# Kernel optimization log

Measured on AMD Instinct MI355X. Metric: run time of the kernel, lower is better.

The kernel has to match this reference:

```python
import jax, jax.numpy as jnp
import numpy as np

BORDER = 8
NMS_THRESH = 0.0
NMS_KSIZE = 5
TOP_K = 512
GAUSS_KSIZE = 15
GAUSS_SIGMA = 0.5
LOSS_LAMBDA = 1.0


def filter_border(x, border=BORDER):
    B, C, H, W = x.shape
    mask = jnp.zeros((H, W), x.dtype).at[border:H - border, border:W - border].set(1.0)
    return x * mask


def _bilinear_sample(img, x, y):
    # img: [H,W]; x,y: [H,W] float pixel coords in src frame; zeros outside.
    H, W = img.shape
    x0 = jnp.floor(x)
    y0 = jnp.floor(y)
    wx1 = x - x0
    wy1 = y - y0

    def gather(yy, xx):
        valid = (xx >= 0) & (xx <= W - 1) & (yy >= 0) & (yy <= H - 1)
        xi = jnp.clip(xx, 0, W - 1).astype(jnp.int32)
        yi = jnp.clip(yy, 0, H - 1).astype(jnp.int32)
        return img[yi, xi] * valid.astype(img.dtype)

    return ((1 - wy1) * (1 - wx1) * gather(y0, x0)
            + (1 - wy1) * wx1 * gather(y0, x0 + 1)
            + wy1 * (1 - wx1) * gather(y0 + 1, x0)
            + wy1 * wx1 * gather(y0 + 1, x0 + 1))


def warp_image(ref, src, homo):
    # Sample src at homo-mapped coords of ref's pixel grid -> output in ref frame.
    B, _, H, W = ref.shape
    ys, xs = jnp.meshgrid(jnp.arange(H, dtype=ref.dtype), jnp.arange(W, dtype=ref.dtype), indexing='ij')
    pts = jnp.stack([xs.ravel(), ys.ravel(), jnp.ones(H * W, ref.dtype)], 0)  # [3, HW]
    mapped = jnp.einsum('bij,jn->bin', homo, pts)  # [B,3,HW]
    x = (mapped[:, 0] / mapped[:, 2]).reshape(B, H, W)
    y = (mapped[:, 1] / mapped[:, 2]).reshape(B, H, W)
    out = jax.vmap(_bilinear_sample)(src[:, 0], x, y)  # [B,H,W]
    return out[:, None]


def select_keypoints(score, thresh, ksize, top_k):
    B, _, H, W = score.shape
    pooled = jax.lax.reduce_window(score, -jnp.inf, jax.lax.max,
                                   (1, 1, ksize, ksize), (1, 1, 1, 1), 'SAME')
    keep = (score == pooled) & (score > thresh)
    s = jnp.where(keep, score, 0.0)
    flat = s.reshape(B, H * W)
    vals, idx = jax.lax.top_k(flat, top_k)
    out = jnp.zeros_like(flat).at[jnp.arange(B)[:, None], idx].set(vals)
    kp = jnp.stack([idx // W, idx % W], -1)  # [B, top_k, 2] (y, x)
    return out.reshape(B, 1, H, W), kp


def gaussian_filter(x, ksize, sigma):
    ax = jnp.arange(ksize, dtype=x.dtype) - (ksize - 1) / 2.0
    g = jnp.exp(-(ax ** 2) / (2.0 * sigma ** 2))
    g = g / g.sum()
    k2 = jnp.outer(g, g)[None, None]  # [1,1,k,k]
    return jax.lax.conv_general_dilated(x, k2, (1, 1), 'SAME')


def setup_inputs() -> dict:
    key = jax.random.key(0)
    k1, k2, k3 = jax.random.split(key, 3)
    B, H, W = 16, 480, 640
    score1 = jax.random.uniform(k1, (B, 1, H, W), jnp.float32)
    score2 = jax.random.uniform(k2, (B, 1, H, W), jnp.float32)
    # Near-identity pixel-space homographies: small rotation/shear/perspective + a few px translation.
    scale = jnp.array([[0.01, 0.01, 2.0],
                       [0.01, 0.01, 2.0],
                       [1e-5, 1e-5, 0.0]], jnp.float32)
    homo12 = jnp.eye(3, dtype=jnp.float32) + jax.random.normal(k3, (B, 3, 3), jnp.float32) * scale
    return {"score1": score1, "score2": score2, "homo12": homo12}


def reference(score1, score2, homo12):
    score2 = filter_border(score2)
    w_score2 = warp_image(score1, score2, homo12)
    vis_mask = jnp.ones_like(score2)
    vis_mask1 = (warp_image(score1, vis_mask, homo12) > 0).astype(score1.dtype)
    s1, kp1 = select_keypoints(score1, NMS_THRESH, NMS_KSIZE, TOP_K)
    s1 = gaussian_filter(s1, GAUSS_KSIZE, GAUSS_SIGMA)
    gt_s1, _ = select_keypoints(w_score2, NMS_THRESH, NMS_KSIZE, TOP_K)
    gt_s1 = gaussian_filter(gt_s1, GAUSS_KSIZE, GAUSS_SIGMA)
    norm = vis_mask1.sum()
    loss = (((s1 - gt_s1) ** 2) * vis_mask1 / norm).sum() * LOSS_LAMBDA
    return (loss, kp1, vis_mask1)
```

## Files before the change

kernel.cpp:

```cpp
#include <hip/hip_runtime.h>
#include <cstdint>
#include <cstddef>

#define BN 16
#define HH 480
#define WW 640
#define HWSZ (HH*WW)
#define CAP 32768
#define TOPK 512
#define RED_BLOCKS 2048
#define NTX 64
#define NTY 16

typedef unsigned long long u64;

#define W2_OFF   0ULL
#define W2_SZ    ((unsigned long long)BN*HWSZ*4ULL)
#define MAPS_OFF (W2_OFF + W2_SZ)
#define MAPS_SZ  (2ULL*BN*HWSZ*4ULL)
#define CAND_OFF (MAPS_OFF + MAPS_SZ)
#define CAND_SZ  (2ULL*BN*CAP*8ULL)
#define CNT_OFF  (CAND_OFF + CAND_SZ)
#define CNT_SZ   (4096ULL)
#define SEL_OFF  (CNT_OFF + CNT_SZ)
#define SEL_SZ   (2ULL*BN*TOPK*8ULL)
#define PART_OFF (SEL_OFF + SEL_SZ)
#define PART_SZ  ((unsigned long long)RED_BLOCKS*2*4ULL)

__global__ void k_warp_vis(const float* __restrict__ score2,
                           const float* __restrict__ homo,
                           float* __restrict__ w2,
                           float* __restrict__ vis) {
    int t = blockIdx.x * 256 + threadIdx.x;
    int b = t / (HWSZ / 4);
    int q = t - b * (HWSZ / 4);
    int p = q * 4;
    int py = p / WW, px = p - py * WW;
    const float* h = homo + b * 9;
    const float* sb = score2 + (size_t)b * HWSZ;

    float4 wout;
    float vout[4];
    #pragma unroll
    for (int u = 0; u < 4; ++u) {
        float fx = (float)(px + u), fy = (float)py;
        float X = h[0] * fx + h[1] * fy + h[2];
        float Y = h[3] * fx + h[4] * fy + h[5];
        float Z = h[6] * fx + h[7] * fy + h[8];
        float x = X / Z, y = Y / Z;
        float x0 = floorf(x), y0 = floorf(y);
        float wx = x - x0, wy = y - y0;
        float vv[4], gv[4];
        #pragma unroll
        for (int j = 0; j < 2; ++j) {
            #pragma unroll
            for (int i = 0; i < 2; ++i) {
                float xx = x0 + (float)i;
                float yy = y0 + (float)j;
                bool valid = (xx >= 0.f) && (xx <= (float)(WW - 1)) &&
                             (yy >= 0.f) && (yy <= (float)(HH - 1));
                int xi = (int)fminf(fmaxf(xx, 0.f), (float)(WW - 1));
                int yi = (int)fminf(fmaxf(yy, 0.f), (float)(HH - 1));
                float v = sb[yi * WW + xi];
                bool inb = (xi >= 8) && (xi < WW - 8) && (yi >= 8) && (yi < HH - 8);
                vv[j * 2 + i] = (valid && inb) ? v : 0.f;
                gv[j * 2 + i] = valid ? 1.f : 0.f;
            }
        }
        float w00 = (1.f - wy) * (1.f - wx), w01 = (1.f - wy) * wx;
        float w10 = wy * (1.f - wx),         w11 = wy * wx;
        float val = w00 * vv[0] + w01 * vv[1] + w10 * vv[2] + w11 * vv[3];
        float vsm = w00 * gv[0] + w01 * gv[1] + w10 * gv[2] + w11 * gv[3];
        ((float*)&wout)[u] = val;
        vout[u] = (vsm > 0.f) ? 1.f : 0.f;
    }
    int base = b * HWSZ + p;
    *reinterpret_cast<float4*>(w2 + base) = wout;
    vis[base + 0] = vout[0];
    vis[base + 1] = vout[1];
    vis[base + 2] = vout[2];
    vis[base + 3] = vout[3];
}

__global__ void k_nms(const float* __restrict__ s1,
                      const float* __restrict__ w2,
                      u64* __restrict__ cand,
                      unsigned int* __restrict__ cnt) {
    __shared__ float tile[NTY + 4][NTX + 4];
    __shared__ float colmax[NTY][NTX + 4];
    __shared__ unsigned int s_loc, s_base;
    int z = blockIdx.z;
    const float* sb = (z < BN) ? (s1 + (size_t)z * HWSZ)
                               : (w2 + (size_t)(z - BN) * HWSZ);
    int tid = threadIdx.x;
    int bx0 = blockIdx.x * NTX, by0 = blockIdx.y * NTY;
    if (tid == 0) s_loc = 0;

    for (int i = tid; i < (NTY + 4) * (NTX + 4); i += 256) {
        int ly = i / (NTX + 4), lx = i - ly * (NTX + 4);
        int gy = by0 + ly - 2, gx = bx0 + lx - 2;
        float v = -__builtin_inff();
        if ((unsigned)gy < (unsigned)HH && (unsigned)gx < (unsigned)WW)
            v = sb[gy * WW + gx];
        tile[ly][lx] = v;
    }
    __syncthreads();

    for (int i = tid; i < NTY * (NTX + 4); i += 256) {
        int y = i / (NTX + 4), x = i - y * (NTX + 4);
        float m = tile[y][x];
        m = fmaxf(m, tile[y + 1][x]);
        m = fmaxf(m, tile[y + 2][x]);
        m = fmaxf(m, tile[y + 3][x]);
        m = fmaxf(m, tile[y + 4][x]);
        colmax[y][x] = m;
    }
    __syncthreads();

    int ox = tid & 63, oyb = (tid >> 6) * 4;
    bool fl[4];
    float vv[4];
    unsigned int pos[4];
    #pragma unroll
    for (int k = 0; k < 4; ++k) {
        int oy = oyb + k;
        float v = tile[oy + 2][ox + 2];
        float m = colmax[oy][ox];
        m = fmaxf(m, colmax[oy][ox + 1]);
        m = fmaxf(m, colmax[oy][ox + 2]);
        m = fmaxf(m, colmax[oy][ox + 3]);
        m = fmaxf(m, colmax[oy][ox + 4]);
        fl[k] = (v == m) && (v > 0.f);
        vv[k] = v;
        if (fl[k]) pos[k] = atomicAdd(&s_loc, 1u);
    }
    __syncthreads();
    if (tid == 0 && s_loc) s_base = atomicAdd(&cnt[z * 32], s_loc);
    __syncthreads();
    #pragma unroll
    for (int k = 0; k < 4; ++k) {
        if (fl[k]) {
            unsigned int off = s_base + pos[k];
            if (off < CAP) {
                int p = (by0 + oyb + k) * WW + bx0 + ox;
                cand[(size_t)z * CAP + off] =
                    ((u64)__float_as_uint(vv[k]) << 32) | (u64)(~(unsigned)p);
            }
        }
    }
}

__global__ __launch_bounds__(1024) void k_topk(const u64* __restrict__ cand,
                                               const unsigned int* __restrict__ cnt,
                                               u64* __restrict__ sel,
                                               float* __restrict__ kp_out) {
    int s = blockIdx.x;
    int tid = threadIdx.x;
    int n = (int)cnt[s * 32];
    if (n > CAP) n = CAP;
    const u64* keys = cand + (size_t)s * CAP;

    __shared__ unsigned int histw[16][256];
    __shared__ unsigned int hist[256];
    __shared__ u64 skeys[TOPK];
    __shared__ int s_digit, s_krem, s_done;
    __shared__ unsigned int s_cnt;

    int wid = tid >> 6;

    if (n > TOPK) {
        u64 prefix = 0ULL;
        int krem = TOPK;
        for (int lvl = 7; lvl >= 0; --lvl) {
            for (int i = tid; i < 16 * 256; i += 1024) ((unsigned int*)histw)[i] = 0u;
            if (tid == 0) s_done = 0;
            __syncthreads();
            int shift = lvl * 8;
            u64 pmask = (lvl == 7) ? 0ULL : (~0ULL << (shift + 8));
            for (int i = tid; i < n; i += 1024) {
                u64 k = keys[i];
                if ((k & pmask) == prefix)
                    atomicAdd(&histw[wid][(unsigned int)((k >> shift) & 0xFF)], 1u);
            }
            __syncthreads();
            if (tid < 256) {
                unsigned int sum = 0;
                #pragma unroll
                for (int w = 0; w < 16; ++w) sum += histw[w][tid];
                hist[tid] = sum;
            }
            __syncthreads();
            for (int off = 1; off < 256; off <<= 1) {
                unsigned int add = 0;
                if (tid < 256 - off) add = hist[tid + off];
                __syncthreads();
                if (tid < 256) hist[tid] += add;
                __syncthreads();
            }
            if (tid < 256) {
                unsigned int ge = hist[tid];
                unsigned int gt = (tid < 255) ? hist[tid + 1] : 0u;
                if (ge >= (unsigned)krem && gt < (unsigned)krem) {
                    s_digit = tid; s_krem = krem - (int)gt;
                    if (ge == (unsigned)krem) s_done = 1;
                }
            }
            __syncthreads();
            prefix |= ((u64)s_digit) << shift;
            krem = s_krem;
            int done = s_done;
            __syncthreads();
            if (done) break;
        }
        if (tid == 0) s_cnt = 0;
        __syncthreads();
        for (int i = tid; i < n; i += 1024) {
            u64 k = keys[i];
            if (k >= prefix) {
                unsigned int pos = atomicAdd(&s_cnt, 1u);
                if (pos < TOPK) skeys[pos] = k;
            }
        }
        __syncthreads();
        for (int i = (int)s_cnt + tid; i < TOPK; i += 1024) skeys[i] = 0ULL;
    } else {
        for (int i = tid; i < TOPK; i += 1024) skeys[i] = (i < n) ? keys[i] : 0ULL;
    }
    __syncthreads();

    for (int k = 2; k <= TOPK; k <<= 1) {
        for (int j = k >> 1; j > 0; j >>= 1) {
            if (tid < 256) {
                int i = (tid % j) + (tid / j) * (j << 1);
                int l = i + j;
                bool desc = ((i & k) == 0);
                u64 a = skeys[i], c = skeys[l];
                if ((a < c) == desc) { skeys[i] = c; skeys[l] = a; }
            }
            __syncthreads();
        }
    }

    int m = s >> 4, b = s & 15;
    for (int i = tid; i < TOPK; i += 1024) {
        u64 k = skeys[i];
        sel[(size_t)s * TOPK + i] = k;
        if (m == 0) {
            unsigned int idx = ~(unsigned int)(k & 0xFFFFFFFFULL);
            int y = (int)(idx / WW), x = (int)(idx - (unsigned int)y * WW);
            kp_out[(size_t)(b * TOPK + i) * 2 + 0] = (float)y;
            kp_out[(size_t)(b * TOPK + i) * 2 + 1] = (float)x;
        }
    }
}

__global__ void k_stamp(const u64* __restrict__ sel,
                        float* __restrict__ maps) {
    int gi = blockIdx.x;
    u64 k = sel[gi];
    float val = __uint_as_float((unsigned int)(k >> 32));
    if (val <= 0.f) return;
    unsigned int idx = ~(unsigned int)(k & 0xFFFFFFFFULL);
    int py = (int)(idx / WW), px = (int)(idx - (unsigned int)py * WW);
    int t = threadIdx.x;
    if (t >= 225) return;
    int dy = t / 15 - 7, dx = t - (dy + 7) * 15 - 7;
    int yy = py + dy, xx = px + dx;
    if (yy < 0 || yy >= HH || xx < 0 || xx >= WW) return;
    const float inv_s2 = 0.61869347f;
    float ga = __expf(-2.f * (float)(dy * dy));
    float gb = __expf(-2.f * (float)(dx * dx));
    int m = gi >> 13, b = (gi >> 9) & 15;
    atomicAdd(&maps[((size_t)m * BN + b) * HWSZ + yy * WW + xx], val * ga * gb * inv_s2);
}

__global__ void k_reduce(const float* __restrict__ maps,
                         const float* __restrict__ vis,
                         float* __restrict__ partial) {
    const int N = BN * HWSZ;
    float lp = 0.f, vsum = 0.f;
    int stride = RED_BLOCKS * 256 * 4;
    for (int i = (blockIdx.x * 256 + threadIdx.x) * 4; i < N; i += stride) {
        float4 m0 = *reinterpret_cast<const float4*>(maps + i);
        float4 m1 = *reinterpret_cast<const float4*>(maps + N + i);
        float v0 = vis[i + 0], v1 = vis[i + 1], v2 = vis[i + 2], v3 = vis[i + 3];
        float d0 = m0.x - m1.x, d1 = m0.y - m1.y, d2 = m0.z - m1.z, d3 = m0.w - m1.w;
        lp += d0 * d0 * v0 + d1 * d1 * v1 + d2 * d2 * v2 + d3 * d3 * v3;
        vsum += v0 + v1 + v2 + v3;
    }
    #pragma unroll
    for (int off = 32; off > 0; off >>= 1) {
        lp   += __shfl_down(lp, off);
        vsum += __shfl_down(vsum, off);
    }
    __shared__ float sl[4], sv[4];
    int w = threadIdx.x >> 6, ln = threadIdx.x & 63;
    if (ln == 0) { sl[w] = lp; sv[w] = vsum; }
    __syncthreads();
    if (threadIdx.x == 0) {
        partial[blockIdx.x * 2 + 0] = sl[0] + sl[1] + sl[2] + sl[3];
        partial[blockIdx.x * 2 + 1] = sv[0] + sv[1] + sv[2] + sv[3];
    }
}

__global__ void k_final(const float* __restrict__ partial, float* __restrict__ out) {
    float a = 0.f, c = 0.f;
    for (int i = threadIdx.x; i < RED_BLOCKS; i += 256) {
        a += partial[i * 2 + 0];
        c += partial[i * 2 + 1];
    }
    #pragma unroll
    for (int off = 32; off > 0; off >>= 1) {
        a += __shfl_down(a, off);
        c += __shfl_down(c, off);
    }
    __shared__ float sl[4], sv[4];
    int w = threadIdx.x >> 6, ln = threadIdx.x & 63;
    if (ln == 0) { sl[w] = a; sv[w] = c; }
    __syncthreads();
    if (threadIdx.x == 0)
        out[0] = (sl[0] + sl[1] + sl[2] + sl[3]) / (sv[0] + sv[1] + sv[2] + sv[3]);
}

extern "C" void kernel_launch(void* const* d_in, const int* in_sizes, int n_in,
                              void* d_out, int out_size, void* d_ws, size_t ws_size,
                              hipStream_t stream) {
    const float* score1 = (const float*)d_in[0];
    const float* score2 = (const float*)d_in[1];
    const float* homo   = (const float*)d_in[2];
    float* out = (float*)d_out;
    char* ws = (char*)d_ws;

    float* w2          = (float*)(ws + W2_OFF);
    float* maps        = (float*)(ws + MAPS_OFF);
    u64* cand          = (u64*)(ws + CAND_OFF);
    unsigned int* cnt  = (unsigned int*)(ws + CNT_OFF);
    u64* sel           = (u64*)(ws + SEL_OFF);
    float* partial     = (float*)(ws + PART_OFF);

    float* kp_out  = out + 1;
    float* vis_out = out + 1 + (size_t)BN * TOPK * 2;

    hipMemsetAsync(maps, 0, MAPS_SZ, stream);
    hipMemsetAsync(cnt, 0, CNT_SZ, stream);

    k_warp_vis<<<BN * HWSZ / (256 * 4), 256, 0, stream>>>(score2, homo, w2, vis_out);

    dim3 g(WW / NTX, HH / NTY, 2 * BN);
    k_nms<<<g, 256, 0, stream>>>(score1, w2, cand, cnt);

    k_topk<<<32, 1024, 0, stream>>>(cand, cnt, sel, kp_out);

    k_stamp<<<2 * BN * TOPK, 256, 0, stream>>>(sel, maps);

    k_reduce<<<RED_BLOCKS, 256, 0, stream>>>(maps, vis_out, partial);
    k_final<<<1, 256, 0, stream>>>(partial, out);
}
```

Before: 213.4 us.

## Skip sorting for stamp maps and double NMS tile height

The top-k kernel now writes the selected keys unsorted straight to global memory. A separate small kernel sorts only the 16 score1 slices, which are needed to emit ordered keypoints, so the bitonic sort is skipped for the warped-score slices that are only stamped. The NMS tile height is also doubled so each thread handles 8 rows, which cuts the halo overhead and the number of blocks. The cost is one extra kernel launch and more registers per NMS thread.

```diff
diff --git a/kernel.cpp b/kernel.cpp
--- a/kernel.cpp
+++ b/kernel.cpp
@@ -10,7 +10,7 @@
 #define TOPK 512
 #define RED_BLOCKS 2048
 #define NTX 64
-#define NTY 16
+#define NTY 32
 
 typedef unsigned long long u64;
 
@@ -117,12 +117,12 @@
     }
     __syncthreads();
 
-    int ox = tid & 63, oyb = (tid >> 6) * 4;
-    bool fl[4];
-    float vv[4];
-    unsigned int pos[4];
-    #pragma unroll
-    for (int k = 0; k < 4; ++k) {
+    int ox = tid & 63, oyb = (tid >> 6) * 8;
+    bool fl[8];
+    float vv[8];
+    unsigned int pos[8];
+    #pragma unroll
+    for (int k = 0; k < 8; ++k) {
         int oy = oyb + k;
         float v = tile[oy + 2][ox + 2];
         float m = colmax[oy][ox];
@@ -138,7 +138,7 @@
     if (tid == 0 && s_loc) s_base = atomicAdd(&cnt[z * 32], s_loc);
     __syncthreads();
     #pragma unroll
-    for (int k = 0; k < 4; ++k) {
+    for (int k = 0; k < 8; ++k) {
         if (fl[k]) {
             unsigned int off = s_base + pos[k];
             if (off < CAP) {
@@ -152,8 +152,7 @@
 
 __global__ __launch_bounds__(1024) void k_topk(const u64* __restrict__ cand,
                                                const unsigned int* __restrict__ cnt,
-                                               u64* __restrict__ sel,
-                                               float* __restrict__ kp_out) {
+                                               u64* __restrict__ sel) {
     int s = blockIdx.x;
     int tid = threadIdx.x;
     int n = (int)cnt[s * 32];
@@ -162,7 +161,6 @@
 
     __shared__ unsigned int histw[16][256];
     __shared__ unsigned int hist[256];
-    __shared__ u64 skeys[TOPK];
     __shared__ int s_digit, s_krem, s_done;
     __shared__ unsigned int s_cnt;
 
@@ -218,39 +216,39 @@
             u64 k = keys[i];
             if (k >= prefix) {
                 unsigned int pos = atomicAdd(&s_cnt, 1u);
-                if (pos < TOPK) skeys[pos] = k;
+                if (pos < TOPK) sel[(size_t)s * TOPK + pos] = k;
             }
         }
         __syncthreads();
-        for (int i = (int)s_cnt + tid; i < TOPK; i += 1024) skeys[i] = 0ULL;
+        for (int i = (int)s_cnt + tid; i < TOPK; i += 1024)
+            sel[(size_t)s * TOPK + i] = 0ULL;
     } else {
-        for (int i = tid; i < TOPK; i += 1024) skeys[i] = (i < n) ? keys[i] : 0ULL;
-    }
-    __syncthreads();
-
+        for (int i = tid; i < TOPK; i += 1024)
+            sel[(size_t)s * TOPK + i] = (i < n) ? keys[i] : 0ULL;
+    }
+}
+
+__global__ void k_sortkp(const u64* __restrict__ sel, float* __restrict__ kp_out) {
+    int b = blockIdx.x;
+    int tid = threadIdx.x;
+    __shared__ u64 sk[TOPK];
+    for (int i = tid; i < TOPK; i += 256) sk[i] = sel[(size_t)b * TOPK + i];
+    __syncthreads();
     for (int k = 2; k <= TOPK; k <<= 1) {
         for (int j = k >> 1; j > 0; j >>= 1) {
-            if (tid < 256) {
-                int i = (tid % j) + (tid / j) * (j << 1);
-                int l = i + j;
-                bool desc = ((i & k) == 0);
-                u64 a = skeys[i], c = skeys[l];
-                if ((a < c) == desc) { skeys[i] = c; skeys[l] = a; }
-            }
-            __syncthreads();
-        }
-    }
-
-    int m = s >> 4, b = s & 15;
-    for (int i = tid; i < TOPK; i += 1024) {
-        u64 k = skeys[i];
-        sel[(size_t)s * TOPK + i] = k;
-        if (m == 0) {
-            unsigned int idx = ~(unsigned int)(k & 0xFFFFFFFFULL);
-            int y = (int)(idx / WW), x = (int)(idx - (unsigned int)y * WW);
-            kp_out[(size_t)(b * TOPK + i) * 2 + 0] = (float)y;
-            kp_out[(size_t)(b * TOPK + i) * 2 + 1] = (float)x;
-        }
+            int i = (tid % j) + (tid / j) * (j << 1);
+            int l = i + j;
+            bool desc = ((i & k) == 0);
+            u64 a = sk[i], c = sk[l];
+            if ((a < c) == desc) { sk[i] = c; sk[l] = a; }
+            __syncthreads();
+        }
+    }
+    for (int i = tid; i < TOPK; i += 256) {
+        unsigned int idx = ~(unsigned int)(sk[i] & 0xFFFFFFFFULL);
+        int y = (int)(idx / WW), x = (int)(idx - (unsigned int)y * WW);
+        kp_out[(size_t)(b * TOPK + i) * 2 + 0] = (float)y;
+        kp_out[(size_t)(b * TOPK + i) * 2 + 1] = (float)x;
     }
 }
 
@@ -349,7 +347,8 @@
     dim3 g(WW / NTX, HH / NTY, 2 * BN);
     k_nms<<<g, 256, 0, stream>>>(score1, w2, cand, cnt);
 
-    k_topk<<<32, 1024, 0, stream>>>(cand, cnt, sel, kp_out);
+    k_topk<<<32, 1024, 0, stream>>>(cand, cnt, sel);
+    k_sortkp<<<16, 256, 0, stream>>>(sel, kp_out);
 
     k_stamp<<<2 * BN * TOPK, 256, 0, stream>>>(sel, maps);
 
```

Result: faster. 205.0 us (-3.9%).
